# Optimization experiments

Measured on AMD Instinct MI355X. Metric: run time of the kernel, lower is better.

Reference implementation:

```python
import jax, jax.numpy as jnp
import numpy as np

N = 100000
NFEAT = 128
NHID = 128
NCLASS = 40
E = 1600000
EPS = 1e-5


def _spmm(vals, src, dst, x, n):
    # y[dst] += vals * x[src]  (sparse adj @ x)
    return jax.ops.segment_sum(vals[:, None] * x[src], dst, num_segments=n)


def _bn(h, gamma, beta, rmean, rvar):
    # BatchNorm1d in eval mode (running statistics)
    return (h - rmean) * jax.lax.rsqrt(rvar + EPS) * gamma + beta


def setup_inputs() -> dict:
    key = jax.random.key(0)
    ks = jax.random.split(key, 24)
    inp = {
        'x': jax.random.normal(ks[0], (N, NFEAT), dtype=jnp.float32),
        'M': jax.random.uniform(ks[1], (N, 1), dtype=jnp.float32),
        'AM': jax.random.uniform(ks[2], (N, 1), dtype=jnp.float32),
        'srcZ': jax.random.randint(ks[3], (E,), 0, N, dtype=jnp.int32),
        'dstZ': jax.random.randint(ks[4], (E,), 0, N, dtype=jnp.int32),
        'valsZ': jax.random.uniform(ks[5], (E,), dtype=jnp.float32),
        'src': jax.random.randint(ks[6], (E,), 0, N, dtype=jnp.int32),
        'dst': jax.random.randint(ks[7], (E,), 0, N, dtype=jnp.int32),
        'vals': jax.random.uniform(ks[8], (E,), dtype=jnp.float32),
        # layer 0 (PaGConv) params
        'W0': jax.random.normal(ks[9], (NHID, NFEAT), dtype=jnp.float32) * (1.414 / np.sqrt(NFEAT)),
        'b0': jnp.zeros((NHID,), dtype=jnp.float32),
        'g0': jnp.ones((NHID,), dtype=jnp.float32),
        'be0': jnp.zeros((NHID,), dtype=jnp.float32),
        'rm0': jax.random.normal(ks[10], (NHID,), dtype=jnp.float32) * 0.1,
        'rv0': jax.random.uniform(ks[11], (NHID,), dtype=jnp.float32) + 0.5,
        # layer 1 (GConv) params
        'W1': jax.random.normal(ks[12], (NHID, NHID), dtype=jnp.float32) * (1.414 / np.sqrt(NHID)),
        'b1': jnp.zeros((NHID,), dtype=jnp.float32),
        'g1': jnp.ones((NHID,), dtype=jnp.float32),
        'be1': jnp.zeros((NHID,), dtype=jnp.float32),
        'rm1': jax.random.normal(ks[13], (NHID,), dtype=jnp.float32) * 0.1,
        'rv1': jax.random.uniform(ks[14], (NHID,), dtype=jnp.float32) + 0.5,
        # layer 2 (GConv) params
        'W2': jax.random.normal(ks[15], (NCLASS, NHID), dtype=jnp.float32) * (1.414 / np.sqrt(NHID)),
        'b2': jnp.zeros((NCLASS,), dtype=jnp.float32),
    }
    return inp


def reference(x, M, AM, srcZ, dstZ, valsZ, src, dst, vals,
              W0, b0, g0, be0, rm0, rv0,
              W1, b1, g1, be1, rm1, rv1,
              W2, b2):
    n = x.shape[0]
    # layer 0: PaGConv with adjZ: fc(spmm(adjZ, M*x) * AM), then BN + ReLU (dropout off in eval)
    h = _spmm(valsZ, srcZ, dstZ, M * x, n) * AM
    h = h @ W0.T + b0
    h = jax.nn.relu(_bn(h, g0, be0, rm0, rv0))
    # layer 1: GConv with adj: fc(spmm(adj, h)), then BN + ReLU
    h = _spmm(vals, src, dst, h, n)
    h = h @ W1.T + b1
    h = jax.nn.relu(_bn(h, g1, be1, rm1, rv1))
    # layer 2: GConv, then log_softmax
    h = _spmm(vals, src, dst, h, n)
    h = h @ W2.T + b2
    return jax.nn.log_softmax(h, axis=-1)
```

## Files before the change

### kernel.cpp

```cpp
#include <hip/hip_runtime.h>
#include <math.h>

#define NFEAT 128
#define NCLS 40
#define NCLSP 64
#define BINROWS 64
#define NBINMAX 1600
#define NBLKC 256
#define CHUNKMAX 6400
#define SEGC 7
#define RSMAX 2048

typedef short bf16x8 __attribute__((ext_vector_type(8)));
typedef float f32x4 __attribute__((ext_vector_type(4)));

__device__ __forceinline__ float bf2f(unsigned int lo16) {
  return __uint_as_float((lo16 & 0xffffu) << 16);
}
__device__ __forceinline__ unsigned int f2bf(float x) {
  unsigned int u = __float_as_uint(x);
  return (u + 0x7fffu + ((u >> 16) & 1u)) >> 16;
}

__global__ void bn_prep(const float* b0, const float* g0, const float* be0,
                        const float* rm0, const float* rv0,
                        const float* b1, const float* g1, const float* be1,
                        const float* rm1, const float* rv1,
                        float* sc0, float* sh0, float* sc1, float* sh1) {
  int t = threadIdx.x;
  if (t < 128) {
    float s = g0[t] * rsqrtf(rv0[t] + 1e-5f);
    sc0[t] = s;
    sh0[t] = (b0[t] - rm0[t]) * s + be0[t];
  } else {
    int i = t - 128;
    float s = g1[i] * rsqrtf(rv1[i] + 1e-5f);
    sc1[i] = s;
    sh1[i] = (b1[i] - rm1[i]) * s + be1[i];
  }
}

__global__ void convert_xm(const float* __restrict__ x, const float* __restrict__ Mv,
                           unsigned short* __restrict__ xm, int n) {
  int i = blockIdx.x * 256 + threadIdx.x;
  if (i >= n * (NFEAT / 8)) return;
  int row = i >> 4;
  float m = Mv[row];
  const float4* p = (const float4*)(x + (size_t)i * 8);
  float4 v0 = p[0], v1 = p[1];
  unsigned int o0 = f2bf(v0.x * m) | (f2bf(v0.y * m) << 16);
  unsigned int o1 = f2bf(v0.z * m) | (f2bf(v0.w * m) << 16);
  unsigned int o2 = f2bf(v1.x * m) | (f2bf(v1.y * m) << 16);
  unsigned int o3 = f2bf(v1.z * m) | (f2bf(v1.w * m) << 16);
  ((uint4*)xm)[i] = make_uint4(o0, o1, o2, o3);
}

__global__ void convert_w(const float* __restrict__ W0, const float* __restrict__ W1,
                          unsigned short* __restrict__ Wb0, unsigned short* __restrict__ Wb1) {
  int i = blockIdx.x * 256 + threadIdx.x;
  const float* W = (i < 2048) ? W0 : W1;
  unsigned short* Wb = (i < 2048) ? Wb0 : Wb1;
  int j = (i < 2048) ? i : i - 2048;
  const float4* p = (const float4*)(W + (size_t)j * 8);
  float4 v0 = p[0], v1 = p[1];
  unsigned int o0 = f2bf(v0.x) | (f2bf(v0.y) << 16);
  unsigned int o1 = f2bf(v0.z) | (f2bf(v0.w) << 16);
  unsigned int o2 = f2bf(v1.x) | (f2bf(v1.y) << 16);
  unsigned int o3 = f2bf(v1.z) | (f2bf(v1.w) << 16);
  ((uint4*)Wb)[j] = make_uint4(o0, o1, o2, o3);
}

__global__ __launch_bounds__(256) void bin_sort1(
    const int* __restrict__ srcp, const int* __restrict__ dstp, const float* __restrict__ valp,
    int2* __restrict__ Drm, int2* __restrict__ binsC, int E, int nbin, int chunk) {
  __shared__ int2 stage[CHUNKMAX];
  __shared__ int cur[NBINMAX];
  __shared__ int ps[256];
  const int t = threadIdx.x, k = blockIdx.x;
  for (int i = t; i < nbin; i += 256) cur[i] = 0;
  __syncthreads();
  const int e0 = k * chunk, e1 = min(E, e0 + chunk);
#pragma unroll 4
  for (int e = e0 + t; e < e1; e += 256) atomicAdd(&cur[dstp[e] >> 6], 1);
  __syncthreads();
  int loc[SEGC], cnt[SEGC];
  int s = 0;
#pragma unroll
  for (int j = 0; j < SEGC; ++j) {
    int i = t * SEGC + j;
    int v = (i < nbin) ? cur[i] : 0;
    loc[j] = s; cnt[j] = v;
    s += v;
  }
  ps[t] = s;
  __syncthreads();
  for (int o = 1; o < 256; o <<= 1) {
    int x = (t >= o) ? ps[t - o] : 0;
    __syncthreads();
    ps[t] += x;
    __syncthreads();
  }
  int ex = ps[t] - s;
#pragma unroll
  for (int j = 0; j < SEGC; ++j) {
    int i = t * SEGC + j;
    if (i < nbin) {
      int o = ex + loc[j];
      Drm[(size_t)k * nbin + i] = make_int2(e0 + o, cnt[j]);
      cur[i] = o;
    }
  }
  __syncthreads();
#pragma unroll 2
  for (int e = e0 + t; e < e1; e += 256) {
    int d = dstp[e];
    int p = atomicAdd(&cur[d >> 6], 1);
    stage[p] = make_int2(srcp[e] | ((d & 63) << 17), __float_as_int(valp[e]));
  }
  __syncthreads();
  const int n = e1 - e0;
  for (int i = t; i < n; i += 256) binsC[e0 + i] = stage[i];
}

__global__ __launch_bounds__(256) void transposeD1(
    const int2* __restrict__ Drm, int2* __restrict__ Dbm, int* __restrict__ binTot, int nbin) {
  __shared__ int2 st[8][256];
  __shared__ int part[256];
  int t = threadIdx.x;
  int i0 = blockIdx.x * 8;
#pragma unroll
  for (int j = 0; j < 8; ++j) {
    int i = i0 + j;
    st[j][t] = (i < nbin) ? Drm[(size_t)t * nbin + i] : make_int2(0, 0);
  }
  __syncthreads();
  {
    int j = t >> 5, ks = (t & 31) * 8;
    int i = i0 + j;
    if (i < nbin) {
      int2* q = &Dbm[(size_t)i * NBLKC + ks];
#pragma unroll
      for (int m = 0; m < 8; ++m) q[m] = st[j][ks + m];
    }
    int p = 0;
#pragma unroll
    for (int m = 0; m < 8; ++m) p += st[j][ks + m].y;
    part[t] = p;
  }
  __syncthreads();
  if (t < 8) {
    int s = 0;
    for (int k = 0; k < 32; ++k) s += part[t * 32 + k];
    if (i0 + t < nbin) binTot[i0 + t] = s;
  }
}

__global__ __launch_bounds__(256) void bin_start1(
    const int* __restrict__ bt, int* __restrict__ bs, int nbin) {
  __shared__ int ps[256];
  int t = threadIdx.x;
  int C = (nbin + 255) / 256;
  int loc[SEGC + 1];
  int sum = 0;
  for (int j = 0; j < C; ++j) {
    int i = t * C + j;
    loc[j] = sum;
    sum += (i < nbin) ? bt[i] : 0;
  }
  ps[t] = sum;
  __syncthreads();
  for (int o = 1; o < 256; o <<= 1) {
    int x = (t >= o) ? ps[t - o] : 0;
    __syncthreads();
    ps[t] += x;
    __syncthreads();
  }
  int ex = ps[t] - sum;
  for (int j = 0; j < C; ++j) {
    int i = t * C + j;
    if (i < nbin) bs[i] = ex + loc[j];
  }
  if (t == 255) bs[nbin] = ps[255];
}

__global__ __launch_bounds__(256) void row_sort(
    const int2* __restrict__ Dbm, const int2* __restrict__ binsC,
    const int* __restrict__ binStart, int2* __restrict__ bins2,
    int* __restrict__ rowptr, int n, int nbin) {
  __shared__ int2 stage[RSMAX];
  __shared__ int ps[256];
  __shared__ int rcnt[BINROWS];
  __shared__ int roff[BINROWS];
  const int b = blockIdx.x, t = threadIdx.x;
  if (t < BINROWS) rcnt[t] = 0;
  int2 run = Dbm[(size_t)b * NBLKC + t];
  ps[t] = run.y;
  __syncthreads();
  for (int o = 1; o < 256; o <<= 1) {
    int x = (t >= o) ? ps[t - o] : 0;
    __syncthreads();
    ps[t] += x;
    __syncthreads();
  }
  int mystart = ps[t] - run.y;
  for (int j = 0; j < run.y; ++j) {
    int2 en = binsC[run.x + j];
    int idx = mystart + j;
    if (idx < RSMAX) stage[idx] = en;
    atomicAdd(&rcnt[(en.x >> 17) & 63], 1);
  }
  __syncthreads();
  const int bs = binStart[b];
  if (t < BINROWS) {
    int c = rcnt[t];
    int s = c;
#pragma unroll
    for (int o = 1; o < 64; o <<= 1) {
      int v = __shfl_up(s, o);
      if (t >= o) s += v;
    }
    int excl = s - c;
    int row = b * BINROWS + t;
    if (row < n) rowptr[row] = bs + excl;
    roff[t] = excl;
  }
  __syncthreads();
  int total = min(ps[255], RSMAX);
  for (int i = t; i < total; i += 256) {
    int2 en = stage[i];
    int row = (en.x >> 17) & 63;
    int p = atomicAdd(&roff[row], 1);
    bins2[bs + p] = en;
  }
  if (b == nbin - 1 && t == 0) rowptr[n] = binStart[nbin];
}

template <bool SCALE>
__global__ __launch_bounds__(256) void spmm128_sorted(
    const int* __restrict__ rowptr, const int2* __restrict__ bins2,
    const unsigned short* __restrict__ X, const float* __restrict__ AM,
    unsigned short* __restrict__ Y, int n) {
  int row = (blockIdx.x * 256 + threadIdx.x) >> 6;
  int lane = threadIdx.x & 63;
  if (row >= n) return;
  int s = rowptr[row], d = rowptr[row + 1] - s;
  int half = lane >> 5, l32 = lane & 31;
  float s0 = 0.f, s1 = 0.f, s2 = 0.f, s3 = 0.f;
  for (int kb = 0; kb < d; kb += 64) {
    int rem = min(64, d - kb);
    int2 my = (lane < rem) ? bins2[s + kb + lane] : make_int2(0, 0);
    int myc = my.x & 0x1FFFF;
    float myw = __int_as_float(my.y);
    for (int k = 0; k < rem; k += 8) {
#pragma unroll
      for (int st = 0; st < 4; ++st) {
        int idx = k + 2 * st + half;
        int c = __shfl(myc, idx);
        float wv = __shfl(myw, idx);
        uint2 pv = *(const uint2*)(X + (size_t)c * NFEAT + l32 * 4);
        s0 += wv * bf2f(pv.x);
        s1 += wv * bf2f(pv.x >> 16);
        s2 += wv * bf2f(pv.y);
        s3 += wv * bf2f(pv.y >> 16);
      }
    }
  }
  s0 += __shfl_xor(s0, 32); s1 += __shfl_xor(s1, 32);
  s2 += __shfl_xor(s2, 32); s3 += __shfl_xor(s3, 32);
  if (SCALE) {
    float am = AM[row];
    s0 *= am; s1 *= am; s2 *= am; s3 *= am;
  }
  unsigned int pk = half ? (f2bf(s2) | (f2bf(s3) << 16)) : (f2bf(s0) | (f2bf(s1) << 16));
  ((unsigned int*)Y)[(size_t)row * (NFEAT / 2) + l32 * 2 + half] = pk;
}

__global__ __launch_bounds__(256) void gemm_mfma128(
    const unsigned short* __restrict__ Y, const unsigned short* __restrict__ Wb,
    const float* __restrict__ scale, const float* __restrict__ shift,
    unsigned short* __restrict__ Out, int M) {
  const int wave = threadIdx.x >> 6;
  const int lane = threadIdx.x & 63;
  const int quad = lane >> 4;
  const int l16 = lane & 15;
  const int arow = blockIdx.x * 64 + wave * 16 + l16;
  const bool rv = arow < M;

  f32x4 acc[8];
#pragma unroll
  for (int c = 0; c < 8; ++c) acc[c] = (f32x4){0.f, 0.f, 0.f, 0.f};

#pragma unroll
  for (int kc = 0; kc < 128; kc += 32) {
    bf16x8 a = rv ? *(const bf16x8*)(Y + (size_t)arow * 128 + kc + quad * 8)
                  : (bf16x8){0, 0, 0, 0, 0, 0, 0, 0};
#pragma unroll
    for (int c = 0; c < 8; ++c) {
      bf16x8 b = *(const bf16x8*)(Wb + (size_t)(c * 16 + l16) * 128 + kc + quad * 8);
      acc[c] = __builtin_amdgcn_mfma_f32_16x16x32_bf16(a, b, acc[c], 0, 0, 0);
    }
  }

  int orow0 = blockIdx.x * 64 + wave * 16 + quad * 4;
#pragma unroll
  for (int c = 0; c < 8; ++c) {
    int col = c * 16 + l16;
    float sc = scale[col], sh = shift[col];
#pragma unroll
    for (int r = 0; r < 4; ++r) {
      int orow = orow0 + r;
      if (orow < M) {
        float v = fmaxf(acc[c][r] * sc + sh, 0.f);
        Out[(size_t)orow * 128 + col] = (unsigned short)f2bf(v);
      }
    }
  }
}

__global__ __launch_bounds__(256) void gemm40_kernel(
    const unsigned short* __restrict__ Y, const float* __restrict__ W,
    unsigned short* __restrict__ G2, int M, int NoutReal) {
  __shared__ float Yt[16][128];
  __shared__ float Bt[16][64];
  const int t = threadIdx.x;
  const int tx = t & 15, ty = t >> 4;
  const int row0 = blockIdx.x * 128;

  float acc[8][4];
#pragma unroll
  for (int i = 0; i < 8; ++i)
#pragma unroll
    for (int j = 0; j < 4; ++j) acc[i][j] = 0.f;

  for (int kc = 0; kc < 128; kc += 16) {
    {
      int r = t >> 1, kh = (t & 1) * 8;
      int gr = row0 + r;
      uint4 v = make_uint4(0, 0, 0, 0);
      if (gr < M) v = *(const uint4*)(Y + (size_t)gr * 128 + kc + kh);
      unsigned int p;
      p = v.x; Yt[kh + 0][r] = bf2f(p); Yt[kh + 1][r] = bf2f(p >> 16);
      p = v.y; Yt[kh + 2][r] = bf2f(p); Yt[kh + 3][r] = bf2f(p >> 16);
      p = v.z; Yt[kh + 4][r] = bf2f(p); Yt[kh + 5][r] = bf2f(p >> 16);
      p = v.w; Yt[kh + 6][r] = bf2f(p); Yt[kh + 7][r] = bf2f(p >> 16);
    }
    {
      int o = t >> 2, kq = t & 3;
      float4 v = make_float4(0.f, 0.f, 0.f, 0.f);
      if (o < NoutReal) v = *(const float4*)&W[(size_t)o * 128 + kc + kq * 4];
      Bt[kq * 4 + 0][o] = v.x; Bt[kq * 4 + 1][o] = v.y;
      Bt[kq * 4 + 2][o] = v.z; Bt[kq * 4 + 3][o] = v.w;
    }
    __syncthreads();
#pragma unroll
    for (int kk = 0; kk < 16; ++kk) {
      float a[8];
      const float4* ap = (const float4*)(&Yt[kk][ty * 8]);
      float4 a0 = ap[0], a1 = ap[1];
      a[0] = a0.x; a[1] = a0.y; a[2] = a0.z; a[3] = a0.w;
      a[4] = a1.x; a[5] = a1.y; a[6] = a1.z; a[7] = a1.w;
      float4 bv = *(const float4*)(&Bt[kk][tx * 4]);
      float b[4] = {bv.x, bv.y, bv.z, bv.w};
#pragma unroll
      for (int i = 0; i < 8; ++i)
#pragma unroll
        for (int j = 0; j < 4; ++j) acc[i][j] += a[i] * b[j];
    }
    __syncthreads();
  }

#pragma unroll
  for (int i = 0; i < 8; ++i) {
    int gr = row0 + ty * 8 + i;
    if (gr < M) {
      uint2 pk;
      pk.x = f2bf(acc[i][0]) | (f2bf(acc[i][1]) << 16);
      pk.y = f2bf(acc[i][2]) | (f2bf(acc[i][3]) << 16);
      *(uint2*)(G2 + (size_t)gr * NCLSP + tx * 4) = pk;
    }
  }
}

__global__ __launch_bounds__(256) void spmm_softmax64(
    const int* __restrict__ rowptr, const int2* __restrict__ bins2,
    const unsigned short* __restrict__ G2, const float* __restrict__ b2,
    float* __restrict__ out, int n) {
  int row = (blockIdx.x * 256 + threadIdx.x) >> 6;
  int lane = threadIdx.x & 63;
  if (row >= n) return;
  const int eidx = lane >> 4, q = lane & 15;
  const bool vq = q < (NCLS / 4);
  float4 bv = vq ? *(const float4*)(b2 + q * 4) : make_float4(0.f, 0.f, 0.f, 0.f);

  int s0i = rowptr[row], d = rowptr[row + 1] - s0i;
  float a0 = 0.f, a1 = 0.f, a2 = 0.f, a3 = 0.f;
  for (int kb = 0; kb < d; kb += 64) {
    int rem = min(64, d - kb);
    int2 my = (lane < rem) ? bins2[s0i + kb + lane] : make_int2(0, 0);
    int myc = my.x & 0x1FFFF;
    float myw = __int_as_float(my.y);
    int steps = (rem + 3) >> 2;
#pragma unroll 4
    for (int st = 0; st < steps; ++st) {
      int idx = st * 4 + eidx;
      int c = __shfl(myc, idx);
      float wv = __shfl(myw, idx);
      uint2 pv = *(const uint2*)(G2 + (size_t)c * NCLSP + q * 4);
      a0 += wv * bf2f(pv.x);
      a1 += wv * bf2f(pv.x >> 16);
      a2 += wv * bf2f(pv.y);
      a3 += wv * bf2f(pv.y >> 16);
    }
  }
  a0 += __shfl_xor(a0, 16); a1 += __shfl_xor(a1, 16);
  a2 += __shfl_xor(a2, 16); a3 += __shfl_xor(a3, 16);
  a0 += __shfl_xor(a0, 32); a1 += __shfl_xor(a1, 32);
  a2 += __shfl_xor(a2, 32); a3 += __shfl_xor(a3, 32);
  float z0 = a0 + bv.x, z1 = a1 + bv.y, z2 = a2 + bv.z, z3 = a3 + bv.w;
  bool par = (eidx == 0) && vq;
  float m = par ? fmaxf(fmaxf(z0, z1), fmaxf(z2, z3)) : -INFINITY;
#pragma unroll
  for (int o = 1; o < 64; o <<= 1) m = fmaxf(m, __shfl_xor(m, o));
  float ex = par ? (__expf(z0 - m) + __expf(z1 - m) + __expf(z2 - m) + __expf(z3 - m)) : 0.f;
#pragma unroll
  for (int o = 1; o < 64; o <<= 1) ex += __shfl_xor(ex, o);
  float lg = m + __logf(ex);
  if (par) {
    *(float4*)&out[(size_t)row * NCLS + q * 4] =
        make_float4(z0 - lg, z1 - lg, z2 - lg, z3 - lg);
  }
}


extern "C" void kernel_launch(void* const* d_in, const int* in_sizes, int n_in,
                              void* d_out, int out_size, void* d_ws, size_t ws_size,
                              hipStream_t stream) {
  const float* x    = (const float*)d_in[0];
  const float* Mv   = (const float*)d_in[1];
  const float* AM   = (const float*)d_in[2];
  const int* srcZ   = (const int*)d_in[3];
  const int* dstZ   = (const int*)d_in[4];
  const float* valsZ= (const float*)d_in[5];
  const int* src    = (const int*)d_in[6];
  const int* dst    = (const int*)d_in[7];
  const float* vals = (const float*)d_in[8];
  const float* W0   = (const float*)d_in[9];
  const float* b0   = (const float*)d_in[10];
  const float* g0   = (const float*)d_in[11];
  const float* be0  = (const float*)d_in[12];
  const float* rm0  = (const float*)d_in[13];
  const float* rv0  = (const float*)d_in[14];
  const float* W1   = (const float*)d_in[15];
  const float* b1   = (const float*)d_in[16];
  const float* g1   = (const float*)d_in[17];
  const float* be1  = (const float*)d_in[18];
  const float* rm1  = (const float*)d_in[19];
  const float* rv1  = (const float*)d_in[20];
  const float* W2   = (const float*)d_in[21];
  const float* b2   = (const float*)d_in[22];
  float* out = (float*)d_out;

  const int N = in_sizes[1];
  const int E = in_sizes[3];
  const int NBIN = (N + BINROWS - 1) / BINROWS;
  const int CHUNK = (E + NBLKC - 1) / NBLKC;

  char* w = (char*)d_ws;
  size_t off = 0;
  auto alloc = [&](size_t bytes) -> void* {
    void* p = w + off;
    off = (off + bytes + 255) & ~(size_t)255;
    return p;
  };
  int2* binsC = (int2*)alloc((size_t)NBLKC * CHUNK * 8);
  int2* Drm = (int2*)alloc((size_t)NBLKC * NBIN * 8);
  int2* Dbm = (int2*)alloc((size_t)NBIN * NBLKC * 8);
  int* binTot = (int*)alloc((size_t)NBIN * 4);
  int* binStart = (int*)alloc((size_t)(NBIN + 1) * 4);
  int2* bins2A = (int2*)alloc((size_t)E * 8);
  int* rowptrA = (int*)alloc((size_t)(N + 1) * 4);
  unsigned short* xm = (unsigned short*)alloc((size_t)N * NFEAT * 2);
  unsigned short* bufA = (unsigned short*)alloc((size_t)N * NFEAT * 2);
  unsigned short* bufB = (unsigned short*)alloc((size_t)N * NFEAT * 2);
  float* sc0 = (float*)alloc(128 * 4);
  float* sh0 = (float*)alloc(128 * 4);
  float* sc1 = (float*)alloc(128 * 4);
  float* sh1 = (float*)alloc(128 * 4);
  unsigned short* Wb0 = (unsigned short*)alloc(128 * 128 * 2);
  unsigned short* Wb1 = (unsigned short*)alloc(128 * 128 * 2);
  int2* bins2Z = (int2*)bufB;
  int* rowptrZ = (int*)((char*)bufB + 13 * 1024 * 1024);
  unsigned short* G2 = bufA;

  const int RB = (N + 3) / 4;
  const int GB64 = (N + 63) / 64;
  const int GB128 = (N + 127) / 128;
  const int TDB = (NBIN + 7) / 8;

  bn_prep<<<1, 256, 0, stream>>>(b0, g0, be0, rm0, rv0, b1, g1, be1, rm1, rv1,
                                 sc0, sh0, sc1, sh1);
  convert_xm<<<(N * (NFEAT / 8) + 255) / 256, 256, 0, stream>>>(x, Mv, xm, N);
  convert_w<<<16, 256, 0, stream>>>(W0, W1, Wb0, Wb1);

  bin_sort1<<<NBLKC, 256, 0, stream>>>(srcZ, dstZ, valsZ, Drm, binsC, E, NBIN, CHUNK);
  transposeD1<<<TDB, 256, 0, stream>>>(Drm, Dbm, binTot, NBIN);
  bin_start1<<<1, 256, 0, stream>>>(binTot, binStart, NBIN);
  row_sort<<<NBIN, 256, 0, stream>>>(Dbm, binsC, binStart, bins2Z, rowptrZ, N, NBIN);

  bin_sort1<<<NBLKC, 256, 0, stream>>>(src, dst, vals, Drm, binsC, E, NBIN, CHUNK);
  transposeD1<<<TDB, 256, 0, stream>>>(Drm, Dbm, binTot, NBIN);
  bin_start1<<<1, 256, 0, stream>>>(binTot, binStart, NBIN);
  row_sort<<<NBIN, 256, 0, stream>>>(Dbm, binsC, binStart, bins2A, rowptrA, N, NBIN);

  spmm128_sorted<true><<<RB, 256, 0, stream>>>(rowptrZ, bins2Z, xm, AM, bufA, N);
  gemm_mfma128<<<GB64, 256, 0, stream>>>(bufA, Wb0, sc0, sh0, bufB, N);

  spmm128_sorted<false><<<RB, 256, 0, stream>>>(rowptrA, bins2A, bufB,
                                                (const float*)nullptr, bufA, N);
  gemm_mfma128<<<GB64, 256, 0, stream>>>(bufA, Wb1, sc1, sh1, bufB, N);

  gemm40_kernel<<<GB128, 256, 0, stream>>>(bufB, W2, G2, N, NCLS);
  spmm_softmax64<<<RB, 256, 0, stream>>>(rowptrA, bins2A, G2, b2, out, N);
}
```

Before: 571.1 us.

## Use MFMA with split-bf16 weights for class GEMM; widen SpMM gathers to 16B

After: 581.6 us. Within noise of the previous version (+1.8%).

```diff
diff --git a/kernel.cpp b/kernel.cpp
--- a/kernel.cpp
+++ b/kernel.cpp
@@ -56,18 +56,42 @@
 }
 
 __global__ void convert_w(const float* __restrict__ W0, const float* __restrict__ W1,
-                          unsigned short* __restrict__ Wb0, unsigned short* __restrict__ Wb1) {
+                          const float* __restrict__ W2,
+                          unsigned short* __restrict__ Wb0, unsigned short* __restrict__ Wb1,
+                          unsigned short* __restrict__ W2hi, unsigned short* __restrict__ W2lo) {
   int i = blockIdx.x * 256 + threadIdx.x;
-  const float* W = (i < 2048) ? W0 : W1;
-  unsigned short* Wb = (i < 2048) ? Wb0 : Wb1;
-  int j = (i < 2048) ? i : i - 2048;
-  const float4* p = (const float4*)(W + (size_t)j * 8);
-  float4 v0 = p[0], v1 = p[1];
-  unsigned int o0 = f2bf(v0.x) | (f2bf(v0.y) << 16);
-  unsigned int o1 = f2bf(v0.z) | (f2bf(v0.w) << 16);
-  unsigned int o2 = f2bf(v1.x) | (f2bf(v1.y) << 16);
-  unsigned int o3 = f2bf(v1.z) | (f2bf(v1.w) << 16);
-  ((uint4*)Wb)[j] = make_uint4(o0, o1, o2, o3);
+  if (i < 4096) {
+    const float* W = (i < 2048) ? W0 : W1;
+    unsigned short* Wb = (i < 2048) ? Wb0 : Wb1;
+    int j = (i < 2048) ? i : i - 2048;
+    const float4* p = (const float4*)(W + (size_t)j * 8);
+    float4 v0 = p[0], v1 = p[1];
+    unsigned int o0 = f2bf(v0.x) | (f2bf(v0.y) << 16);
+    unsigned int o1 = f2bf(v0.z) | (f2bf(v0.w) << 16);
+    unsigned int o2 = f2bf(v1.x) | (f2bf(v1.y) << 16);
+    unsigned int o3 = f2bf(v1.z) | (f2bf(v1.w) << 16);
+    ((uint4*)Wb)[j] = make_uint4(o0, o1, o2, o3);
+  } else {
+    int j = i - 4096;
+    int r = j >> 4;
+    float v[8] = {0.f, 0.f, 0.f, 0.f, 0.f, 0.f, 0.f, 0.f};
+    if (r < NCLS) {
+      const float4* p = (const float4*)(W2 + (size_t)j * 8);
+      float4 a = p[0], b = p[1];
+      v[0] = a.x; v[1] = a.y; v[2] = a.z; v[3] = a.w;
+      v[4] = b.x; v[5] = b.y; v[6] = b.z; v[7] = b.w;
+    }
+    unsigned int h[8], l[8];
+#pragma unroll
+    for (int q = 0; q < 8; ++q) {
+      h[q] = f2bf(v[q]);
+      l[q] = f2bf(v[q] - bf2f(h[q]));
+    }
+    ((uint4*)W2hi)[j] = make_uint4(h[0] | (h[1] << 16), h[2] | (h[3] << 16),
+                                   h[4] | (h[5] << 16), h[6] | (h[7] << 16));
+    ((uint4*)W2lo)[j] = make_uint4(l[0] | (l[1] << 16), l[2] | (l[3] << 16),
+                                   l[4] | (l[5] << 16), l[6] | (l[7] << 16));
+  }
 }
 
 __global__ __launch_bounds__(256) void bin_sort1(
@@ -244,35 +268,48 @@
   int lane = threadIdx.x & 63;
   if (row >= n) return;
   int s = rowptr[row], d = rowptr[row + 1] - s;
-  int half = lane >> 5, l32 = lane & 31;
-  float s0 = 0.f, s1 = 0.f, s2 = 0.f, s3 = 0.f;
+  int eidx = lane >> 4, l16 = lane & 15;
+  float acc[8] = {0.f, 0.f, 0.f, 0.f, 0.f, 0.f, 0.f, 0.f};
   for (int kb = 0; kb < d; kb += 64) {
     int rem = min(64, d - kb);
     int2 my = (lane < rem) ? bins2[s + kb + lane] : make_int2(0, 0);
     int myc = my.x & 0x1FFFF;
     float myw = __int_as_float(my.y);
-    for (int k = 0; k < rem; k += 8) {
-#pragma unroll
-      for (int st = 0; st < 4; ++st) {
-        int idx = k + 2 * st + half;
-        int c = __shfl(myc, idx);
-        float wv = __shfl(myw, idx);
-        uint2 pv = *(const uint2*)(X + (size_t)c * NFEAT + l32 * 4);
-        s0 += wv * bf2f(pv.x);
-        s1 += wv * bf2f(pv.x >> 16);
-        s2 += wv * bf2f(pv.y);
-        s3 += wv * bf2f(pv.y >> 16);
-      }
-    }
-  }
-  s0 += __shfl_xor(s0, 32); s1 += __shfl_xor(s1, 32);
-  s2 += __shfl_xor(s2, 32); s3 += __shfl_xor(s3, 32);
+    int steps = (rem + 3) >> 2;
+#pragma unroll 4
+    for (int st = 0; st < steps; ++st) {
+      int idx = st * 4 + eidx;
+      int c = __shfl(myc, idx);
+      float wv = __shfl(myw, idx);
+      uint4 pv = *(const uint4*)(X + (size_t)c * NFEAT + l16 * 8);
+      acc[0] += wv * bf2f(pv.x);
+      acc[1] += wv * bf2f(pv.x >> 16);
+      acc[2] += wv * bf2f(pv.y);
+      acc[3] += wv * bf2f(pv.y >> 16);
+      acc[4] += wv * bf2f(pv.z);
+      acc[5] += wv * bf2f(pv.z >> 16);
+      acc[6] += wv * bf2f(pv.w);
+      acc[7] += wv * bf2f(pv.w >> 16);
+    }
+  }
+#pragma unroll
+  for (int j = 0; j < 8; ++j) {
+    acc[j] += __shfl_xor(acc[j], 16);
+    acc[j] += __shfl_xor(acc[j], 32);
+  }
   if (SCALE) {
     float am = AM[row];
-    s0 *= am; s1 *= am; s2 *= am; s3 *= am;
-  }
-  unsigned int pk = half ? (f2bf(s2) | (f2bf(s3) << 16)) : (f2bf(s0) | (f2bf(s1) << 16));
-  ((unsigned int*)Y)[(size_t)row * (NFEAT / 2) + l32 * 2 + half] = pk;
+#pragma unroll
+    for (int j = 0; j < 8; ++j) acc[j] *= am;
+  }
+  if (eidx == 0) {
+    uint4 pk;
+    pk.x = f2bf(acc[0]) | (f2bf(acc[1]) << 16);
+    pk.y = f2bf(acc[2]) | (f2bf(acc[3]) << 16);
+    pk.z = f2bf(acc[4]) | (f2bf(acc[5]) << 16);
+    pk.w = f2bf(acc[6]) | (f2bf(acc[7]) << 16);
+    *(uint4*)(Y + (size_t)row * NFEAT + l16 * 8) = pk;
+  }
 }
 
 __global__ __launch_bounds__(256) void gemm_mfma128(
@@ -317,66 +354,41 @@
   }
 }
 
-__global__ __launch_bounds__(256) void gemm40_kernel(
-    const unsigned short* __restrict__ Y, const float* __restrict__ W,
-    unsigned short* __restrict__ G2, int M, int NoutReal) {
-  __shared__ float Yt[16][128];
-  __shared__ float Bt[16][64];
-  const int t = threadIdx.x;
-  const int tx = t & 15, ty = t >> 4;
-  const int row0 = blockIdx.x * 128;
-
-  float acc[8][4];
-#pragma unroll
-  for (int i = 0; i < 8; ++i)
-#pragma unroll
-    for (int j = 0; j < 4; ++j) acc[i][j] = 0.f;
-
-  for (int kc = 0; kc < 128; kc += 16) {
-    {
-      int r = t >> 1, kh = (t & 1) * 8;
-      int gr = row0 + r;
-      uint4 v = make_uint4(0, 0, 0, 0);
-      if (gr < M) v = *(const uint4*)(Y + (size_t)gr * 128 + kc + kh);
-      unsigned int p;
-      p = v.x; Yt[kh + 0][r] = bf2f(p); Yt[kh + 1][r] = bf2f(p >> 16);
-      p = v.y; Yt[kh + 2][r] = bf2f(p); Yt[kh + 3][r] = bf2f(p >> 16);
-      p = v.z; Yt[kh + 4][r] = bf2f(p); Yt[kh + 5][r] = bf2f(p >> 16);
-      p = v.w; Yt[kh + 6][r] = bf2f(p); Yt[kh + 7][r] = bf2f(p >> 16);
-    }
-    {
-      int o = t >> 2, kq = t & 3;
-      float4 v = make_float4(0.f, 0.f, 0.f, 0.f);
-      if (o < NoutReal) v = *(const float4*)&W[(size_t)o * 128 + kc + kq * 4];
-      Bt[kq * 4 + 0][o] = v.x; Bt[kq * 4 + 1][o] = v.y;
-      Bt[kq * 4 + 2][o] = v.z; Bt[kq * 4 + 3][o] = v.w;
-    }
-    __syncthreads();
-#pragma unroll
-    for (int kk = 0; kk < 16; ++kk) {
-      float a[8];
-      const float4* ap = (const float4*)(&Yt[kk][ty * 8]);
-      float4 a0 = ap[0], a1 = ap[1];
-      a[0] = a0.x; a[1] = a0.y; a[2] = a0.z; a[3] = a0.w;
-      a[4] = a1.x; a[5] = a1.y; a[6] = a1.z; a[7] = a1.w;
-      float4 bv = *(const float4*)(&Bt[kk][tx * 4]);
-      float b[4] = {bv.x, bv.y, bv.z, bv.w};
-#pragma unroll
-      for (int i = 0; i < 8; ++i)
-#pragma unroll
-        for (int j = 0; j < 4; ++j) acc[i][j] += a[i] * b[j];
-    }
-    __syncthreads();
-  }
-
-#pragma unroll
-  for (int i = 0; i < 8; ++i) {
-    int gr = row0 + ty * 8 + i;
-    if (gr < M) {
-      uint2 pk;
-      pk.x = f2bf(acc[i][0]) | (f2bf(acc[i][1]) << 16);
-      pk.y = f2bf(acc[i][2]) | (f2bf(acc[i][3]) << 16);
-      *(uint2*)(G2 + (size_t)gr * NCLSP + tx * 4) = pk;
+__global__ __launch_bounds__(256) void gemm40_mfma(
+    const unsigned short* __restrict__ Y, const unsigned short* __restrict__ Whi,
+    const unsigned short* __restrict__ Wlo, unsigned short* __restrict__ G2, int M) {
+  const int wave = threadIdx.x >> 6;
+  const int lane = threadIdx.x & 63;
+  const int quad = lane >> 4;
+  const int l16 = lane & 15;
+  const int arow = blockIdx.x * 64 + wave * 16 + l16;
+  const bool rv = arow < M;
+
+  f32x4 acc[4];
+#pragma unroll
+  for (int c = 0; c < 4; ++c) acc[c] = (f32x4){0.f, 0.f, 0.f, 0.f};
+
+#pragma unroll
+  for (int kc = 0; kc < 128; kc += 32) {
+    bf16x8 a = rv ? *(const bf16x8*)(Y + (size_t)arow * 128 + kc + quad * 8)
+                  : (bf16x8){0, 0, 0, 0, 0, 0, 0, 0};
+#pragma unroll
+    for (int c = 0; c < 4; ++c) {
+      bf16x8 bh = *(const bf16x8*)(Whi + (size_t)(c * 16 + l16) * 128 + kc + quad * 8);
+      bf16x8 bl = *(const bf16x8*)(Wlo + (size_t)(c * 16 + l16) * 128 + kc + quad * 8);
+      acc[c] = __builtin_amdgcn_mfma_f32_16x16x32_bf16(a, bh, acc[c], 0, 0, 0);
+      acc[c] = __builtin_amdgcn_mfma_f32_16x16x32_bf16(a, bl, acc[c], 0, 0, 0);
+    }
+  }
+
+  int orow0 = blockIdx.x * 64 + wave * 16 + quad * 4;
+#pragma unroll
+  for (int c = 0; c < 4; ++c) {
+    int col = c * 16 + l16;
+#pragma unroll
+    for (int r = 0; r < 4; ++r) {
+      int orow = orow0 + r;
+      if (orow < M) G2[(size_t)orow * NCLSP + col] = (unsigned short)f2bf(acc[c][r]);
     }
   }
 }
@@ -388,46 +400,68 @@
   int row = (blockIdx.x * 256 + threadIdx.x) >> 6;
   int lane = threadIdx.x & 63;
   if (row >= n) return;
-  const int eidx = lane >> 4, q = lane & 15;
-  const bool vq = q < (NCLS / 4);
-  float4 bv = vq ? *(const float4*)(b2 + q * 4) : make_float4(0.f, 0.f, 0.f, 0.f);
+  const int eidx = lane >> 3, oct = lane & 7;
+  const bool vq = oct < (NCLS / 8);
+  float4 bv0 = make_float4(0.f, 0.f, 0.f, 0.f), bv1 = bv0;
+  if (vq) {
+    bv0 = *(const float4*)(b2 + oct * 8);
+    bv1 = *(const float4*)(b2 + oct * 8 + 4);
+  }
 
   int s0i = rowptr[row], d = rowptr[row + 1] - s0i;
-  float a0 = 0.f, a1 = 0.f, a2 = 0.f, a3 = 0.f;
+  float a[8] = {0.f, 0.f, 0.f, 0.f, 0.f, 0.f, 0.f, 0.f};
   for (int kb = 0; kb < d; kb += 64) {
     int rem = min(64, d - kb);
     int2 my = (lane < rem) ? bins2[s0i + kb + lane] : make_int2(0, 0);
     int myc = my.x & 0x1FFFF;
     float myw = __int_as_float(my.y);
-    int steps = (rem + 3) >> 2;
-#pragma unroll 4
+    int steps = (rem + 7) >> 3;
+#pragma unroll 2
     for (int st = 0; st < steps; ++st) {
-      int idx = st * 4 + eidx;
+      int idx = st * 8 + eidx;
       int c = __shfl(myc, idx);
       float wv = __shfl(myw, idx);
-      uint2 pv = *(const uint2*)(G2 + (size_t)c * NCLSP + q * 4);
-      a0 += wv * bf2f(pv.x);
-      a1 += wv * bf2f(pv.x >> 16);
-      a2 += wv * bf2f(pv.y);
-      a3 += wv * bf2f(pv.y >> 16);
-    }
-  }
-  a0 += __shfl_xor(a0, 16); a1 += __shfl_xor(a1, 16);
-  a2 += __shfl_xor(a2, 16); a3 += __shfl_xor(a3, 16);
-  a0 += __shfl_xor(a0, 32); a1 += __shfl_xor(a1, 32);
-  a2 += __shfl_xor(a2, 32); a3 += __shfl_xor(a3, 32);
-  float z0 = a0 + bv.x, z1 = a1 + bv.y, z2 = a2 + bv.z, z3 = a3 + bv.w;
+      uint4 pv = *(const uint4*)(G2 + (size_t)c * NCLSP + oct * 8);
+      a[0] += wv * bf2f(pv.x);
+      a[1] += wv * bf2f(pv.x >> 16);
+      a[2] += wv * bf2f(pv.y);
+      a[3] += wv * bf2f(pv.y >> 16);
+      a[4] += wv * bf2f(pv.z);
+      a[5] += wv * bf2f(pv.z >> 16);
+      a[6] += wv * bf2f(pv.w);
+      a[7] += wv * bf2f(pv.w >> 16);
+    }
+  }
+#pragma unroll
+  for (int j = 0; j < 8; ++j) {
+    a[j] += __shfl_xor(a[j], 8);
+    a[j] += __shfl_xor(a[j], 16);
+    a[j] += __shfl_xor(a[j], 32);
+  }
+  float z[8];
+  z[0] = a[0] + bv0.x; z[1] = a[1] + bv0.y; z[2] = a[2] + bv0.z; z[3] = a[3] + bv0.w;
+  z[4] = a[4] + bv1.x; z[5] = a[5] + bv1.y; z[6] = a[6] + bv1.z; z[7] = a[7] + bv1.w;
   bool par = (eidx == 0) && vq;
-  float m = par ? fmaxf(fmaxf(z0, z1), fmaxf(z2, z3)) : -INFINITY;
+  float m = -INFINITY;
+  if (par) {
+    m = fmaxf(fmaxf(fmaxf(z[0], z[1]), fmaxf(z[2], z[3])),
+              fmaxf(fmaxf(z[4], z[5]), fmaxf(z[6], z[7])));
+  }
 #pragma unroll
   for (int o = 1; o < 64; o <<= 1) m = fmaxf(m, __shfl_xor(m, o));
-  float ex = par ? (__expf(z0 - m) + __expf(z1 - m) + __expf(z2 - m) + __expf(z3 - m)) : 0.f;
+  float ex = 0.f;
+  if (par) {
+#pragma unroll
+    for (int j = 0; j < 8; ++j) ex += __expf(z[j] - m);
+  }
 #pragma unroll
   for (int o = 1; o < 64; o <<= 1) ex += __shfl_xor(ex, o);
   float lg = m + __logf(ex);
   if (par) {
-    *(float4*)&out[(size_t)row * NCLS + q * 4] =
-        make_float4(z0 - lg, z1 - lg, z2 - lg, z3 - lg);
+    *(float4*)&out[(size_t)row * NCLS + oct * 8] =
+        make_float4(z[0] - lg, z[1] - lg, z[2] - lg, z[3] - lg);
+    *(float4*)&out[(size_t)row * NCLS + oct * 8 + 4] =
+        make_float4(z[4] - lg, z[5] - lg, z[6] - lg, z[7] - lg);
   }
 }
 
@@ -488,19 +522,20 @@
   float* sh1 = (float*)alloc(128 * 4);
   unsigned short* Wb0 = (unsigned short*)alloc(128 * 128 * 2);
   unsigned short* Wb1 = (unsigned short*)alloc(128 * 128 * 2);
+  unsigned short* W2hi = (unsigned short*)alloc(64 * 128 * 2);
+  unsigned short* W2lo = (unsigned short*)alloc(64 * 128 * 2);
   int2* bins2Z = (int2*)bufB;
   int* rowptrZ = (int*)((char*)bufB + 13 * 1024 * 1024);
   unsigned short* G2 = bufA;
 
   const int RB = (N + 3) / 4;
   const int GB64 = (N + 63) / 64;
-  const int GB128 = (N + 127) / 128;
   const int TDB = (NBIN + 7) / 8;
 
   bn_prep<<<1, 256, 0, stream>>>(b0, g0, be0, rm0, rv0, b1, g1, be1, rm1, rv1,
                                  sc0, sh0, sc1, sh1);
   convert_xm<<<(N * (NFEAT / 8) + 255) / 256, 256, 0, stream>>>(x, Mv, xm, N);
-  convert_w<<<16, 256, 0, stream>>>(W0, W1, Wb0, Wb1);
+  convert_w<<<20, 256, 0, stream>>>(W0, W1, W2, Wb0, Wb1, W2hi, W2lo);
 
   bin_sort1<<<NBLKC, 256, 0, stream>>>(srcZ, dstZ, valsZ, Drm, binsC, E, NBIN, CHUNK);
   transposeD1<<<TDB, 256, 0, stream>>>(Drm, Dbm, binTot, NBIN);
@@ -519,6 +554,6 @@
                                                 (const float*)nullptr, bufA, N);
   gemm_mfma128<<<GB64, 256, 0, stream>>>(bufA, Wb1, sc1, sh1, bufB, N);
 
-  gemm40_kernel<<<GB128, 256, 0, stream>>>(bufB, W2, G2, N, NCLS);
+  gemm40_mfma<<<GB64, 256, 0, stream>>>(bufB, W2hi, W2lo, G2, N);
   spmm_softmax64<<<RB, 256, 0, stream>>>(rowptrA, bins2A, G2, b2, out, N);
 }
```
